# Performance work log

Hardware: AMD Instinct MI355X
Metric: run time of the kernel (lower is better)

Reference implementation:

```python
import jax, jax.numpy as jnp
import numpy as np

N_NODES = 100000
N_EDGES = 1600000
N_GRAPHS = 64
D_IN = 3
HIDDEN = 256
N_CLASSES = 10
NEG_SLOPE = 0.01  # torch F.leaky_relu default


def gcn_conv(x, W, b, src, dst, n_nodes):
    """GCNConv: D^{-1/2}(A+I)D^{-1/2} X W + b with self-loops."""
    h = x @ W  # [N, H]
    ones = jnp.ones(src.shape[0], h.dtype)
    deg = jax.ops.segment_sum(ones, dst, num_segments=n_nodes) + 1.0  # +1 self-loop
    dinv = jax.lax.rsqrt(deg)
    coef = dinv[src] * dinv[dst]  # [E]
    agg = jax.ops.segment_sum(h[src] * coef[:, None], dst, num_segments=n_nodes)
    agg = agg + h * (1.0 / deg)[:, None]  # self-loop contribution (norm = 1/deg)
    return agg + b


def leaky_relu(v):
    return jnp.where(v >= 0, v, NEG_SLOPE * v)


def setup_inputs() -> dict:
    key = jax.random.key(0)
    ks = jax.random.split(key, 12)
    x = jax.random.normal(ks[0], (N_NODES, D_IN), dtype=jnp.float32)
    edge_index = jax.random.randint(ks[1], (2, N_EDGES), 0, N_NODES, dtype=jnp.int32)
    batch = jnp.sort(jax.random.randint(ks[2], (N_NODES,), 0, N_GRAPHS, dtype=jnp.int32))
    s1 = 1.0 / np.sqrt(D_IN)
    s2 = 1.0 / np.sqrt(HIDDEN)
    W1 = jax.random.uniform(ks[3], (D_IN, HIDDEN), jnp.float32, -s1, s1)
    b1 = jnp.zeros((HIDDEN,), jnp.float32)
    W2 = jax.random.uniform(ks[4], (HIDDEN, HIDDEN), jnp.float32, -s2, s2)
    b2 = jnp.zeros((HIDDEN,), jnp.float32)
    W3 = jax.random.uniform(ks[5], (HIDDEN, HIDDEN), jnp.float32, -s2, s2)
    b3 = jnp.zeros((HIDDEN,), jnp.float32)
    Wc = jax.random.uniform(ks[6], (HIDDEN, N_CLASSES), jnp.float32, -s2, s2)
    bc = jax.random.uniform(ks[7], (N_CLASSES,), jnp.float32, -s2, s2)
    return {"x": x, "edge_index": edge_index, "batch": batch,
            "W1": W1, "b1": b1, "W2": W2, "b2": b2, "W3": W3, "b3": b3,
            "Wc": Wc, "bc": bc}


def reference(x, edge_index, batch, W1, b1, W2, b2, W3, b3, Wc, bc):
    src, dst = edge_index[0], edge_index[1]
    h = leaky_relu(gcn_conv(x, W1, b1, src, dst, N_NODES))
    h = leaky_relu(gcn_conv(h, W2, b2, src, dst, N_NODES))
    h = leaky_relu(gcn_conv(h, W3, b3, src, dst, N_NODES))
    # global mean pool over graphs
    sums = jax.ops.segment_sum(h, batch, num_segments=N_GRAPHS)
    cnt = jax.ops.segment_sum(jnp.ones((N_NODES,), h.dtype), batch, num_segments=N_GRAPHS)
    pooled = sums / jnp.maximum(cnt, 1.0)[:, None]  # [G, H]
    logits = pooled @ Wc + bc
    return jax.nn.softmax(logits, axis=1)
```

## Files before the change

### kernel.cpp

```cpp
#include <hip/hip_runtime.h>
#include <hip/hip_bf16.h>
#include <hip/hip_fp16.h>
#include <cstdint>
#include <cstddef>

#define N_NODES   100000
#define N_EDGES   1600000
#define N_GRAPHS  64
#define HIDDEN    256
#define N_CLASSES 10
#define NEG_SLOPE 0.01f

#define E_PAD    (N_EDGES + 8 * N_NODES)
#define GEMM_BLOCKS 391

#define PART_EDGES  8192
#define PART_BLOCKS ((N_EDGES + PART_EDGES - 1) / PART_EDGES)
#define SUB_BITS 10
#define SUB_SIZE 1024
#define N_SUB    ((N_NODES + SUB_SIZE - 1) / SUB_SIZE)
#define CAP_SUB  17408

typedef __attribute__((ext_vector_type(4))) float f32x4;
typedef __attribute__((ext_vector_type(2))) float f32x2;

__device__ __forceinline__ float bf2f(unsigned short u) {
    return __uint_as_float(((unsigned int)u) << 16);
}

__device__ __forceinline__ unsigned char f2fp8(float v) {
    return (unsigned char)(__builtin_amdgcn_cvt_pk_fp8_f32(v, v, 0, false) & 0xff);
}

__device__ __forceinline__ unsigned int rec_pack(int s, float c) {
    __half h = __float2half(c);
    unsigned short hb = reinterpret_cast<const __half_raw*>(&h)->x;
    return ((unsigned int)hb << 17) | (unsigned int)s;
}
__device__ __forceinline__ float rec_coef(unsigned int u) {
    __half_raw hr; hr.x = (unsigned short)(u >> 17);
    return __half2float(*reinterpret_cast<const __half*>(&hr));
}

__global__ __launch_bounds__(256) void k_partition(const int* __restrict__ src, const int* __restrict__ dst,
                                                   int* __restrict__ gcur, unsigned int* __restrict__ bucket) {
    __shared__ int lcnt[N_SUB];
    __shared__ int lbase[N_SUB];
    __shared__ int gbase[N_SUB];
    __shared__ unsigned int stage[PART_EDGES];
    int tid = threadIdx.x;
    for (int i = tid; i < N_SUB; i += 256) lcnt[i] = 0;
    __syncthreads();
    int e0 = blockIdx.x * PART_EDGES + tid * 8;
    for (int g = 0; g < 4; ++g) {
        int e = e0 + g * 2048;
        if (e < N_EDGES) {
            int4 da = *(const int4*)(dst + e);
            int4 db = *(const int4*)(dst + e + 4);
            int d[8] = {da.x, da.y, da.z, da.w, db.x, db.y, db.z, db.w};
#pragma unroll
            for (int j = 0; j < 8; ++j) atomicAdd(&lcnt[d[j] >> SUB_BITS], 1);
        }
    }
    __syncthreads();
    if (tid == 0) {
        int s = 0;
        for (int r = 0; r < N_SUB; ++r) { lbase[r] = s; s += lcnt[r]; }
    }
    __syncthreads();
    for (int i = tid; i < N_SUB; i += 256) {
        gbase[i] = atomicAdd(&gcur[i * 16], lcnt[i]);
        lcnt[i] = lbase[i];
    }
    __syncthreads();
    for (int g = 0; g < 4; ++g) {
        int e = e0 + g * 2048;
        if (e < N_EDGES) {
            int4 da = *(const int4*)(dst + e);
            int4 db = *(const int4*)(dst + e + 4);
            int4 sa = *(const int4*)(src + e);
            int4 sb = *(const int4*)(src + e + 4);
            int d[8] = {da.x, da.y, da.z, da.w, db.x, db.y, db.z, db.w};
            int s[8] = {sa.x, sa.y, sa.z, sa.w, sb.x, sb.y, sb.z, sb.w};
#pragma unroll
            for (int j = 0; j < 8; ++j) {
                int r = d[j] >> SUB_BITS;
                int p = atomicAdd(&lcnt[r], 1);
                stage[p] = ((unsigned int)(d[j] & (SUB_SIZE - 1)) << 17) | (unsigned int)s[j];
            }
        }
    }
    __syncthreads();
    int wv = tid >> 6, ln = tid & 63;
    for (int r = wv; r < N_SUB; r += 4) {
        int base = lbase[r], n = lcnt[r] - base, gb = gbase[r];
        unsigned int* dp = bucket + (size_t)r * CAP_SUB + gb;
        for (int k = ln; k < n; k += 64) dp[k] = stage[base + k];
    }
}

__global__ __launch_bounds__(512) void k_hist3(const unsigned int* __restrict__ bucket,
                                               const int* __restrict__ gcur, int* __restrict__ cnt) {
    int sub = blockIdx.x;
    __shared__ int hist[SUB_SIZE];
    for (int i = threadIdx.x; i < SUB_SIZE; i += 512) hist[i] = 0;
    __syncthreads();
    int n = gcur[sub * 16];
    const unsigned int* bp = bucket + (size_t)sub * CAP_SUB;
    for (int i0 = threadIdx.x * 8; i0 < n; i0 += 512 * 8) {
        uint4 ua = *(const uint4*)(bp + i0);
        uint4 ub = *(const uint4*)(bp + i0 + 4);
        unsigned int u[8] = {ua.x, ua.y, ua.z, ua.w, ub.x, ub.y, ub.z, ub.w};
        int m = n - i0; if (m > 8) m = 8;
#pragma unroll
        for (int j = 0; j < 8; ++j) if (j < m) atomicAdd(&hist[u[j] >> 17], 1);
    }
    __syncthreads();
    int base = sub * SUB_SIZE;
    for (int i = threadIdx.x; i < SUB_SIZE; i += 512)
        if (base + i < N_NODES) cnt[base + i] = hist[i];
}

__global__ __launch_bounds__(512) void k_fill3(const unsigned int* __restrict__ bucket,
                                               const int* __restrict__ gcur,
                                               const float* __restrict__ dinv,
                                               const int* __restrict__ off,
                                               unsigned int* __restrict__ rec) {
    int sub = blockIdx.x;
    __shared__ int lcur[SUB_SIZE];
    __shared__ float ldv[SUB_SIZE];
    int nb0 = sub * SUB_SIZE;
    for (int i = threadIdx.x; i < SUB_SIZE; i += 512) {
        int node = nb0 + i;
        lcur[i] = (node < N_NODES) ? off[node] : 0;
        ldv[i]  = (node < N_NODES) ? dinv[node] : 0.f;
    }
    __syncthreads();
    int n = gcur[sub * 16];
    const unsigned int* bp = bucket + (size_t)sub * CAP_SUB;
    for (int i0 = threadIdx.x * 8; i0 < n; i0 += 512 * 8) {
        uint4 ua = *(const uint4*)(bp + i0);
        uint4 ub = *(const uint4*)(bp + i0 + 4);
        unsigned int u[8] = {ua.x, ua.y, ua.z, ua.w, ub.x, ub.y, ub.z, ub.w};
        int m = n - i0; if (m > 8) m = 8;
        float ds[8];
#pragma unroll
        for (int j = 0; j < 8; ++j) {
            int s = (j < m) ? (int)(u[j] & 0x1ffff) : 0;
            ds[j] = dinv[s];
        }
#pragma unroll
        for (int j = 0; j < 8; ++j) {
            if (j < m) {
                int dr = (int)(u[j] >> 17);
                float c = ds[j] * ldv[dr];
                int p = atomicAdd(&lcur[dr], 1);
                rec[p] = rec_pack((int)(u[j] & 0x1ffff), c);
            }
        }
    }
}

__global__ void k_graph_bounds(const int* __restrict__ batch,
                               int* __restrict__ gstart, int* __restrict__ gcnt) {
    int g = threadIdx.x;
    int lo = 0, hi = N_NODES;
    while (lo < hi) { int mid = (lo + hi) >> 1; if (batch[mid] < g) lo = mid + 1; else hi = mid; }
    __shared__ int sh[N_GRAPHS + 1];
    sh[g] = lo;
    if (g == 0) sh[N_GRAPHS] = N_NODES;
    __syncthreads();
    gstart[g] = sh[g];
    gcnt[g]   = sh[g + 1] - sh[g];
}

__global__ void k_dinv_xpad(const int* __restrict__ cnt, const float* __restrict__ x,
                            float* __restrict__ dinv, float4* __restrict__ xp) {
    int i = blockIdx.x * 256 + threadIdx.x;
    if (i < N_NODES) {
        dinv[i] = rsqrtf((float)cnt[i] + 1.0f);
        xp[i] = make_float4(x[i * 3 + 0], x[i * 3 + 1], x[i * 3 + 2], 0.f);
    }
}

__global__ void k_scanA(const int* __restrict__ cnt, int* __restrict__ out, int* __restrict__ bsum) {
    __shared__ int sh[256];
    int tid = threadIdx.x;
    int base = blockIdx.x * 1024 + tid * 4;
    int v[4]; int s = 0;
#pragma unroll
    for (int i = 0; i < 4; i++) {
        int idx = base + i;
        v[i] = (idx < N_NODES) ? ((cnt[idx] + 7) & ~7) : 0;
        s += v[i];
    }
    sh[tid] = s; __syncthreads();
    for (int off = 1; off < 256; off <<= 1) {
        int t = (tid >= off) ? sh[tid - off] : 0;
        __syncthreads();
        sh[tid] += t;
        __syncthreads();
    }
    int excl = sh[tid] - s;
    if (tid == 255) bsum[blockIdx.x] = sh[255];
#pragma unroll
    for (int i = 0; i < 4; i++) { int idx = base + i; if (idx < N_NODES) out[idx] = excl; excl += v[i]; }
}

__global__ void k_scanB(int* __restrict__ bsum, int nb) {
    __shared__ int sh[128];
    int tid = threadIdx.x;
    int v = (tid < nb) ? bsum[tid] : 0;
    sh[tid] = v; __syncthreads();
    for (int off = 1; off < 128; off <<= 1) {
        int t = (tid >= off) ? sh[tid - off] : 0;
        __syncthreads();
        sh[tid] += t;
        __syncthreads();
    }
    if (tid < nb) bsum[tid] = sh[tid] - v;
}

__global__ void k_scanC(int* __restrict__ off_arr, const int* __restrict__ bsum,
                        const int* __restrict__ cnt, unsigned int* __restrict__ rec) {
    int i = blockIdx.x * 256 + threadIdx.x;
    if (i < N_NODES) {
        int v = off_arr[i] + bsum[i >> 10];
        off_arr[i] = v;
        int c  = cnt[i];
        int cp = (c + 7) & ~7;
        for (int p = v + c; p < v + cp; ++p) rec[p] = 0u;
        if (i == N_NODES - 1) off_arr[N_NODES] = v + cp;
    }
}

__global__ void k_wprep(const float* __restrict__ W, unsigned char* __restrict__ Wswz) {
    int n = blockIdx.x; int k = threadIdx.x;
    unsigned char v = f2fp8(W[k * HIDDEN + n]);
    int k0 = k >> 5, nt = n >> 4;
    int lane = (((k >> 3) & 3) << 4) | (n & 15);
    int j = k & 7;
    Wswz[(size_t)(((k0 * 16) + nt) * 64 + lane) * 8 + j] = v;
}

__global__ void k_agg3(const float4* __restrict__ xp, const int* __restrict__ off,
                       const unsigned int* __restrict__ rec, const float* __restrict__ dinv,
                       float4* __restrict__ ax) {
    int i = blockIdx.x * 256 + threadIdx.x;
    if (i >= N_NODES) return;
    float di = dinv[i];
    float selfc = di * di;
    float4 xi = xp[i];
    float a0 = xi.x * selfc, a1 = xi.y * selfc, a2 = xi.z * selfc;
    int e = off[i], e1 = off[i + 1];
    for (; e < e1; e += 4) {
        uint4 rr = *(const uint4*)(rec + e);
        int s0 = rr.x & 0x1ffff, s1 = rr.y & 0x1ffff, s2 = rr.z & 0x1ffff, s3 = rr.w & 0x1ffff;
        float c0 = rec_coef(rr.x), c1 = rec_coef(rr.y), c2 = rec_coef(rr.z), c3 = rec_coef(rr.w);
        float4 x0 = xp[s0], x1 = xp[s1], x2 = xp[s2], x3 = xp[s3];
        a0 += c0 * x0.x + c1 * x1.x + c2 * x2.x + c3 * x3.x;
        a1 += c0 * x0.y + c1 * x1.y + c2 * x2.y + c3 * x3.y;
        a2 += c0 * x0.z + c1 * x1.z + c2 * x2.z + c3 * x3.z;
    }
    ax[i] = make_float4(a0, a1, a2, 0.f);
}

__global__ void k_l1(const float4* __restrict__ ax, const float* __restrict__ W1,
                     const float* __restrict__ b1, unsigned char* __restrict__ out) {
    int node = blockIdx.x; int c = threadIdx.x;
    float4 a = ax[node];
    float v = a.x * W1[c] + a.y * W1[HIDDEN + c] + a.z * W1[2 * HIDDEN + c] + b1[c];
    v = v >= 0.f ? v : NEG_SLOPE * v;
    out[(size_t)node * HIDDEN + c] = f2fp8(v);
}

__global__ __launch_bounds__(512, 2) void k_gemm_mfma(const unsigned char* __restrict__ A,
                                                      const unsigned char* __restrict__ Wswz,
                                                      unsigned char* __restrict__ C, int M) {
    __shared__ long Bs[8192];
    __shared__ unsigned int St[8][320];
    int tid = threadIdx.x;
    {
        const float4* gsrc = (const float4*)Wswz;
        float4* ldst = (float4*)Bs;
#pragma unroll
        for (int i = 0; i < 8; ++i) ldst[tid + 512 * i] = gsrc[tid + 512 * i];
    }
    __syncthreads();
    int lane = tid & 63, wv = tid >> 6;
    int quad = lane >> 4, r = lane & 15;
    int nstrips = M >> 4;
    unsigned int* stw = &St[wv][0];
    int rrow = lane >> 2, rseg = lane & 3;
    for (int s = blockIdx.x * 8 + wv; s < nstrips; s += GEMM_BLOCKS * 8) {
        int m0 = s * 16;
        const long* Ab = (const long*)(A + (size_t)(m0 + r) * HIDDEN) + quad;
        long af[8];
#pragma unroll
        for (int k0 = 0; k0 < 8; ++k0) af[k0] = Ab[k0 * 4];
        f32x4 acc[16];
#pragma unroll
        for (int i = 0; i < 16; i++) acc[i] = (f32x4){0.f, 0.f, 0.f, 0.f};
#pragma unroll
        for (int k0 = 0; k0 < 8; ++k0) {
#pragma unroll
            for (int nt = 0; nt < 16; ++nt) {
                long w = Bs[(k0 * 16 + nt) * 64 + lane];
                acc[nt] = __builtin_amdgcn_mfma_f32_16x16x32_fp8_fp8(w, af[k0], acc[nt], 0, 0, 0);
            }
        }
#pragma unroll
        for (int q4 = 0; q4 < 4; ++q4) {
#pragma unroll
            for (int t = 0; t < 4; ++t) {
                f32x4 a = acc[q4 * 4 + t];
                unsigned int pk = __builtin_amdgcn_cvt_pk_fp8_f32(a[0], a[1], 0, false);
                pk = __builtin_amdgcn_cvt_pk_fp8_f32(a[2], a[3], pk, true);
                stw[r * 20 + t * 4 + quad] = pk;
            }
            uint4 v = *(const uint4*)&stw[rrow * 20 + rseg * 4];
            *(uint4*)(C + (size_t)(m0 + rrow) * HIDDEN + q4 * 64 + rseg * 16) = v;
        }
    }
}

__global__ __launch_bounds__(256) void k_agg(const unsigned char* __restrict__ h,
                                             const float* __restrict__ bias,
                                             const int* __restrict__ off, const unsigned int* __restrict__ rec,
                                             const float* __restrict__ dinv,
                                             unsigned char* __restrict__ out) {
    int node = (blockIdx.x * 256 + threadIdx.x) >> 6;
    int lane = threadIdx.x & 63;
    if (node >= N_NODES) return;
    float di = dinv[node];
    float selfc = di * di;
    unsigned int hv = *(const unsigned int*)(h + (size_t)node * HIDDEN + lane * 4);
    f32x2 hlo = __builtin_amdgcn_cvt_pk_f32_fp8(hv, false);
    f32x2 hhi = __builtin_amdgcn_cvt_pk_f32_fp8(hv, true);
    float4 bv = ((const float4*)bias)[lane];
    float4 acc = make_float4(bv.x + hlo.x * selfc, bv.y + hlo.y * selfc,
                             bv.z + hhi.x * selfc, bv.w + hhi.y * selfc);
    int e = off[node], e1 = off[node + 1];
    for (; e < e1; e += 8) {
        uint4 ra = *(const uint4*)(rec + e);
        uint4 rb = *(const uint4*)(rec + e + 4);
        unsigned int w0 = *(const unsigned int*)(h + (size_t)(ra.x & 0x1ffff) * HIDDEN + lane * 4);
        unsigned int w1 = *(const unsigned int*)(h + (size_t)(ra.y & 0x1ffff) * HIDDEN + lane * 4);
        unsigned int w2 = *(const unsigned int*)(h + (size_t)(ra.z & 0x1ffff) * HIDDEN + lane * 4);
        unsigned int w3 = *(const unsigned int*)(h + (size_t)(ra.w & 0x1ffff) * HIDDEN + lane * 4);
        unsigned int w4 = *(const unsigned int*)(h + (size_t)(rb.x & 0x1ffff) * HIDDEN + lane * 4);
        unsigned int w5 = *(const unsigned int*)(h + (size_t)(rb.y & 0x1ffff) * HIDDEN + lane * 4);
        unsigned int w6 = *(const unsigned int*)(h + (size_t)(rb.z & 0x1ffff) * HIDDEN + lane * 4);
        unsigned int w7 = *(const unsigned int*)(h + (size_t)(rb.w & 0x1ffff) * HIDDEN + lane * 4);
        float c0 = rec_coef(ra.x), c1 = rec_coef(ra.y), c2 = rec_coef(ra.z), c3 = rec_coef(ra.w);
        float c4 = rec_coef(rb.x), c5 = rec_coef(rb.y), c6 = rec_coef(rb.z), c7 = rec_coef(rb.w);
        f32x2 l0 = __builtin_amdgcn_cvt_pk_f32_fp8(w0, false), g0 = __builtin_amdgcn_cvt_pk_f32_fp8(w0, true);
        f32x2 l1 = __builtin_amdgcn_cvt_pk_f32_fp8(w1, false), g1 = __builtin_amdgcn_cvt_pk_f32_fp8(w1, true);
        f32x2 l2 = __builtin_amdgcn_cvt_pk_f32_fp8(w2, false), g2 = __builtin_amdgcn_cvt_pk_f32_fp8(w2, true);
        f32x2 l3 = __builtin_amdgcn_cvt_pk_f32_fp8(w3, false), g3 = __builtin_amdgcn_cvt_pk_f32_fp8(w3, true);
        f32x2 l4 = __builtin_amdgcn_cvt_pk_f32_fp8(w4, false), g4 = __builtin_amdgcn_cvt_pk_f32_fp8(w4, true);
        f32x2 l5 = __builtin_amdgcn_cvt_pk_f32_fp8(w5, false), g5 = __builtin_amdgcn_cvt_pk_f32_fp8(w5, true);
        f32x2 l6 = __builtin_amdgcn_cvt_pk_f32_fp8(w6, false), g6 = __builtin_amdgcn_cvt_pk_f32_fp8(w6, true);
        f32x2 l7 = __builtin_amdgcn_cvt_pk_f32_fp8(w7, false), g7 = __builtin_amdgcn_cvt_pk_f32_fp8(w7, true);
        acc.x += c0 * l0.x + c1 * l1.x + c2 * l2.x + c3 * l3.x
               + c4 * l4.x + c5 * l5.x + c6 * l6.x + c7 * l7.x;
        acc.y += c0 * l0.y + c1 * l1.y + c2 * l2.y + c3 * l3.y
               + c4 * l4.y + c5 * l5.y + c6 * l6.y + c7 * l7.y;
        acc.z += c0 * g0.x + c1 * g1.x + c2 * g2.x + c3 * g3.x
               + c4 * g4.x + c5 * g5.x + c6 * g6.x + c7 * g7.x;
        acc.w += c0 * g0.y + c1 * g1.y + c2 * g2.y + c3 * g3.y
               + c4 * g4.y + c5 * g5.y + c6 * g6.y + c7 * g7.y;
    }
    acc.x = acc.x >= 0.f ? acc.x : NEG_SLOPE * acc.x;
    acc.y = acc.y >= 0.f ? acc.y : NEG_SLOPE * acc.y;
    acc.z = acc.z >= 0.f ? acc.z : NEG_SLOPE * acc.z;
    acc.w = acc.w >= 0.f ? acc.w : NEG_SLOPE * acc.w;
    unsigned int pk = __builtin_amdgcn_cvt_pk_fp8_f32(acc.x, acc.y, 0, false);
    pk = __builtin_amdgcn_cvt_pk_fp8_f32(acc.z, acc.w, pk, true);
    *(unsigned int*)(out + (size_t)node * HIDDEN + lane * 4) = pk;
}

__global__ void k_pool(const unsigned char* __restrict__ h, const int* __restrict__ gstart,
                       const int* __restrict__ gcnt, float* __restrict__ pooled) {
    int g = blockIdx.x, chunk = blockIdx.y, t = threadIdx.x;
    int s = gstart[g], c = gcnt[g];
    int i0 = s + (int)(((long long)c * chunk) / 16);
    int i1 = s + (int)(((long long)c * (chunk + 1)) / 16);
    float acc = 0.f;
    for (int i = i0; i < i1; ++i) {
        f32x2 v = __builtin_amdgcn_cvt_pk_f32_fp8((unsigned int)h[(size_t)i * HIDDEN + t], false);
        acc += v.x;
    }
    atomicAdd(&pooled[g * HIDDEN + t], acc);
}

__global__ void k_head(const float* __restrict__ pooled, const int* __restrict__ gcnt,
                       const float* __restrict__ Wc, const float* __restrict__ bc,
                       float* __restrict__ out) {
    int g = blockIdx.x; int l = threadIdx.x;
    float inv = 1.0f / fmaxf((float)gcnt[g], 1.0f);
    float p[4];
#pragma unroll
    for (int i = 0; i < 4; i++) p[i] = pooled[g * HIDDEN + l + i * 64] * inv;
    __shared__ float logits[N_CLASSES];
#pragma unroll
    for (int j = 0; j < N_CLASSES; j++) {
        float s = 0.f;
#pragma unroll
        for (int i = 0; i < 4; i++) s += p[i] * Wc[(l + i * 64) * N_CLASSES + j];
        for (int o = 32; o > 0; o >>= 1) s += __shfl_down(s, o, 64);
        if (l == 0) logits[j] = s + bc[j];
    }
    __syncthreads();
    if (l == 0) {
        float m = logits[0];
        for (int j = 1; j < N_CLASSES; j++) m = fmaxf(m, logits[j]);
        float e[N_CLASSES]; float sum = 0.f;
        for (int j = 0; j < N_CLASSES; j++) { e[j] = expf(logits[j] - m); sum += e[j]; }
        for (int j = 0; j < N_CLASSES; j++) out[g * N_CLASSES + j] = e[j] / sum;
    }
}

extern "C" void kernel_launch(void* const* d_in, const int* in_sizes, int n_in,
                              void* d_out, int out_size, void* d_ws, size_t ws_size,
                              hipStream_t stream) {
    const float* x     = (const float*)d_in[0];
    const int*   edge  = (const int*)d_in[1];
    const int*   batch = (const int*)d_in[2];
    const float* W1 = (const float*)d_in[3];
    const float* b1 = (const float*)d_in[4];
    const float* W2 = (const float*)d_in[5];
    const float* b2 = (const float*)d_in[6];
    const float* W3 = (const float*)d_in[7];
    const float* b3 = (const float*)d_in[8];
    const float* Wc = (const float*)d_in[9];
    const float* bc = (const float*)d_in[10];
    float* out = (float*)d_out;
    const int* srcp = edge;
    const int* dstp = edge + N_EDGES;

    char* ws = (char*)d_ws;
    size_t off = 0;
    auto alloc = [&](size_t bytes) -> char* {
        char* p = ws + off;
        off += (bytes + 255) & ~(size_t)255;
        return p;
    };
    unsigned char* hA   = (unsigned char*)alloc((size_t)N_NODES * HIDDEN);
    unsigned char* hB   = (unsigned char*)alloc((size_t)N_NODES * HIDDEN);
    unsigned char* Wz2  = (unsigned char*)alloc((size_t)HIDDEN * HIDDEN);
    unsigned char* Wz3  = (unsigned char*)alloc((size_t)HIDDEN * HIDDEN);
    int*   deg_cnt  = (int*)alloc((size_t)N_NODES * 4);
    float* dinv     = (float*)alloc((size_t)N_NODES * 4);
    int*   csr_off  = (int*)alloc((size_t)(N_NODES + 1) * 4);
    unsigned int* csr_rec = (unsigned int*)alloc((size_t)E_PAD * 4);
    float4* ax      = (float4*)alloc((size_t)N_NODES * 16);
    float4* xp      = (float4*)alloc((size_t)N_NODES * 16);
    int*   gcnt     = (int*)alloc((size_t)N_GRAPHS * 4);
    int*   gstart   = (int*)alloc((size_t)N_GRAPHS * 4);
    float* pooled   = (float*)alloc((size_t)N_GRAPHS * HIDDEN * 4);
    int*   bsum     = (int*)alloc(128 * 4);
    int*   gcur     = (int*)alloc((size_t)N_SUB * 16 * 4);

    unsigned int* bucket = (unsigned int*)hB;

    hipMemsetAsync(gcur, 0, (size_t)N_SUB * 16 * 4, stream);
    hipMemsetAsync(pooled, 0, (size_t)N_GRAPHS * HIDDEN * 4, stream);

    int nb  = (N_NODES + 255) / 256;
    int sblocks = (N_NODES + 1023) / 1024;

    k_partition<<<PART_BLOCKS, 256, 0, stream>>>(srcp, dstp, gcur, bucket);
    k_graph_bounds<<<1, 64, 0, stream>>>(batch, gstart, gcnt);
    k_hist3<<<N_SUB, 512, 0, stream>>>(bucket, gcur, deg_cnt);
    k_dinv_xpad<<<nb, 256, 0, stream>>>(deg_cnt, x, dinv, xp);
    k_scanA<<<sblocks, 256, 0, stream>>>(deg_cnt, csr_off, bsum);
    k_scanB<<<1, 128, 0, stream>>>(bsum, sblocks);
    k_scanC<<<nb, 256, 0, stream>>>(csr_off, bsum, deg_cnt, csr_rec);
    k_fill3<<<N_SUB, 512, 0, stream>>>(bucket, gcur, dinv, csr_off, csr_rec);
    k_wprep<<<HIDDEN, HIDDEN, 0, stream>>>(W2, Wz2);
    k_wprep<<<HIDDEN, HIDDEN, 0, stream>>>(W3, Wz3);

    k_agg3<<<nb, 256, 0, stream>>>(xp, csr_off, csr_rec, dinv, ax);
    k_l1<<<N_NODES, 256, 0, stream>>>(ax, W1, b1, hA);

    int aggb = (N_NODES + 3) / 4;
    k_gemm_mfma<<<GEMM_BLOCKS, 512, 0, stream>>>(hA, Wz2, hB, N_NODES);
    k_agg<<<aggb, 256, 0, stream>>>(hB, b2, csr_off, csr_rec, dinv, hA);
    k_gemm_mfma<<<GEMM_BLOCKS, 512, 0, stream>>>(hA, Wz3, hB, N_NODES);
    k_agg<<<aggb, 256, 0, stream>>>(hB, b3, csr_off, csr_rec, dinv, hA);
    dim3 pg(N_GRAPHS, 16);
    k_pool<<<pg, 256, 0, stream>>>(hA, gstart, gcnt, pooled);
    k_head<<<N_GRAPHS, 64, 0, stream>>>(pooled, gcnt, Wc, bc, out);
}
```

Before: 455.7 us.

## Fuse dinv/xpad into hist, degree-sort layer-1 aggregation, batch k_l1 and wprep

Folds the dinv and padded-x computation into the histogram kernel and merges the two weight-prep launches into one, removing launches. Adds a per-1024-node counting sort by degree so the first-layer aggregation threads in a wavefront have similar edge counts, which is meant to reduce divergence. It also rewrites k_l1 to handle 32 nodes per block with W1 and b1 staged in shared memory instead of one block per node. The cost is an extra sort kernel and a perm array, plus scattered writes to ax.

```diff
diff --git a/kernel.cpp b/kernel.cpp
--- a/kernel.cpp
+++ b/kernel.cpp
@@ -100,7 +100,9 @@
 }
 
 __global__ __launch_bounds__(512) void k_hist3(const unsigned int* __restrict__ bucket,
-                                               const int* __restrict__ gcur, int* __restrict__ cnt) {
+                                               const int* __restrict__ gcur, int* __restrict__ cnt,
+                                               const float* __restrict__ x,
+                                               float* __restrict__ dinv, float4* __restrict__ xp) {
     int sub = blockIdx.x;
     __shared__ int hist[SUB_SIZE];
     for (int i = threadIdx.x; i < SUB_SIZE; i += 512) hist[i] = 0;
@@ -117,8 +119,44 @@
     }
     __syncthreads();
     int base = sub * SUB_SIZE;
-    for (int i = threadIdx.x; i < SUB_SIZE; i += 512)
-        if (base + i < N_NODES) cnt[base + i] = hist[i];
+    for (int i = threadIdx.x; i < SUB_SIZE; i += 512) {
+        int node = base + i;
+        if (node < N_NODES) {
+            int c = hist[i];
+            cnt[node] = c;
+            dinv[node] = rsqrtf((float)c + 1.0f);
+            xp[node] = make_float4(x[node * 3 + 0], x[node * 3 + 1], x[node * 3 + 2], 0.f);
+        }
+    }
+}
+
+__global__ __launch_bounds__(512) void k_locsort(const int* __restrict__ cnt, int* __restrict__ perm) {
+    int sub = blockIdx.x, t = threadIdx.x;
+    __shared__ int hist[256];
+    __shared__ int curs[256];
+    if (t < 256) hist[t] = 0;
+    __syncthreads();
+    int base = sub * SUB_SIZE;
+    int i0 = base + t, i1 = base + t + 512;
+    int d0 = -1, d1 = -1;
+    if (i0 < N_NODES) { d0 = min(cnt[i0], 254); atomicAdd(&hist[d0], 1); }
+    if (i1 < N_NODES) { d1 = min(cnt[i1], 254); atomicAdd(&hist[d1], 1); }
+    __syncthreads();
+    if (t < 256) curs[t] = hist[t];
+    __syncthreads();
+    for (int off = 1; off < 256; off <<= 1) {
+        int v = 0;
+        if (t < 256 && t >= off) v = curs[t - off];
+        __syncthreads();
+        if (t < 256) curs[t] += v;
+        __syncthreads();
+    }
+    if (t < 256) curs[t] -= hist[t];
+    __syncthreads();
+    if (d0 >= 0) { int p = atomicAdd(&curs[d0], 1); perm[base + p] = i0; }
+    if (d1 >= 0) { int p = atomicAdd(&curs[d1], 1); perm[base + p] = i1; }
+    int nvalid = N_NODES - base; if (nvalid > SUB_SIZE) nvalid = SUB_SIZE;
+    for (int k = nvalid + t; k < SUB_SIZE; k += 512) perm[base + k] = 0x7fffffff;
 }
 
 __global__ __launch_bounds__(512) void k_fill3(const unsigned int* __restrict__ bucket,
@@ -174,15 +212,6 @@
     gcnt[g]   = sh[g + 1] - sh[g];
 }
 
-__global__ void k_dinv_xpad(const int* __restrict__ cnt, const float* __restrict__ x,
-                            float* __restrict__ dinv, float4* __restrict__ xp) {
-    int i = blockIdx.x * 256 + threadIdx.x;
-    if (i < N_NODES) {
-        dinv[i] = rsqrtf((float)cnt[i] + 1.0f);
-        xp[i] = make_float4(x[i * 3 + 0], x[i * 3 + 1], x[i * 3 + 2], 0.f);
-    }
-}
-
 __global__ void k_scanA(const int* __restrict__ cnt, int* __restrict__ out, int* __restrict__ bsum) {
     __shared__ int sh[256];
     int tid = threadIdx.x;
@@ -234,7 +263,10 @@
     }
 }
 
-__global__ void k_wprep(const float* __restrict__ W, unsigned char* __restrict__ Wswz) {
+__global__ void k_wprep2(const float* __restrict__ W2, const float* __restrict__ W3,
+                         unsigned char* __restrict__ Wz2, unsigned char* __restrict__ Wz3) {
+    const float* W = blockIdx.y ? W3 : W2;
+    unsigned char* Wswz = blockIdx.y ? Wz3 : Wz2;
     int n = blockIdx.x; int k = threadIdx.x;
     unsigned char v = f2fp8(W[k * HIDDEN + n]);
     int k0 = k >> 5, nt = n >> 4;
@@ -245,8 +277,9 @@
 
 __global__ void k_agg3(const float4* __restrict__ xp, const int* __restrict__ off,
                        const unsigned int* __restrict__ rec, const float* __restrict__ dinv,
-                       float4* __restrict__ ax) {
-    int i = blockIdx.x * 256 + threadIdx.x;
+                       const int* __restrict__ perm, float4* __restrict__ ax) {
+    int gid = blockIdx.x * 256 + threadIdx.x;
+    int i = perm[gid];
     if (i >= N_NODES) return;
     float di = dinv[i];
     float selfc = di * di;
@@ -265,13 +298,22 @@
     ax[i] = make_float4(a0, a1, a2, 0.f);
 }
 
-__global__ void k_l1(const float4* __restrict__ ax, const float* __restrict__ W1,
-                     const float* __restrict__ b1, unsigned char* __restrict__ out) {
-    int node = blockIdx.x; int c = threadIdx.x;
-    float4 a = ax[node];
-    float v = a.x * W1[c] + a.y * W1[HIDDEN + c] + a.z * W1[2 * HIDDEN + c] + b1[c];
-    v = v >= 0.f ? v : NEG_SLOPE * v;
-    out[(size_t)node * HIDDEN + c] = f2fp8(v);
+__global__ __launch_bounds__(256) void k_l1(const float4* __restrict__ ax, const float* __restrict__ W1,
+                                            const float* __restrict__ b1, unsigned char* __restrict__ out) {
+    __shared__ float w0s[HIDDEN], w1s[HIDDEN], w2s[HIDDEN], bbs[HIDDEN];
+    int t = threadIdx.x;
+    w0s[t] = W1[t]; w1s[t] = W1[HIDDEN + t]; w2s[t] = W1[2 * HIDDEN + t]; bbs[t] = b1[t];
+    __syncthreads();
+    int base = blockIdx.x * 32;
+#pragma unroll 4
+    for (int i = 0; i < 32; ++i) {
+        int node = base + i;
+        if (node >= N_NODES) break;
+        float4 a = ax[node];
+        float v = a.x * w0s[t] + a.y * w1s[t] + a.z * w2s[t] + bbs[t];
+        v = v >= 0.f ? v : NEG_SLOPE * v;
+        out[(size_t)node * HIDDEN + t] = f2fp8(v);
+    }
 }
 
 __global__ __launch_bounds__(512, 2) void k_gemm_mfma(const unsigned char* __restrict__ A,
@@ -461,6 +503,7 @@
     float* pooled   = (float*)alloc((size_t)N_GRAPHS * HIDDEN * 4);
     int*   bsum     = (int*)alloc(128 * 4);
     int*   gcur     = (int*)alloc((size_t)N_SUB * 16 * 4);
+    int*   perm     = (int*)alloc((size_t)N_SUB * SUB_SIZE * 4);
 
     unsigned int* bucket = (unsigned int*)hB;
 
@@ -472,17 +515,17 @@
 
     k_partition<<<PART_BLOCKS, 256, 0, stream>>>(srcp, dstp, gcur, bucket);
     k_graph_bounds<<<1, 64, 0, stream>>>(batch, gstart, gcnt);
-    k_hist3<<<N_SUB, 512, 0, stream>>>(bucket, gcur, deg_cnt);
-    k_dinv_xpad<<<nb, 256, 0, stream>>>(deg_cnt, x, dinv, xp);
+    k_hist3<<<N_SUB, 512, 0, stream>>>(bucket, gcur, deg_cnt, x, dinv, xp);
+    k_locsort<<<N_SUB, 512, 0, stream>>>(deg_cnt, perm);
     k_scanA<<<sblocks, 256, 0, stream>>>(deg_cnt, csr_off, bsum);
     k_scanB<<<1, 128, 0, stream>>>(bsum, sblocks);
     k_scanC<<<nb, 256, 0, stream>>>(csr_off, bsum, deg_cnt, csr_rec);
     k_fill3<<<N_SUB, 512, 0, stream>>>(bucket, gcur, dinv, csr_off, csr_rec);
-    k_wprep<<<HIDDEN, HIDDEN, 0, stream>>>(W2, Wz2);
-    k_wprep<<<HIDDEN, HIDDEN, 0, stream>>>(W3, Wz3);
-
-    k_agg3<<<nb, 256, 0, stream>>>(xp, csr_off, csr_rec, dinv, ax);
-    k_l1<<<N_NODES, 256, 0, stream>>>(ax, W1, b1, hA);
+    dim3 wg(HIDDEN, 2);
+    k_wprep2<<<wg, HIDDEN, 0, stream>>>(W2, W3, Wz2, Wz3);
+
+    k_agg3<<<(N_SUB * SUB_SIZE) / 256, 256, 0, stream>>>(xp, csr_off, csr_rec, dinv, perm, ax);
+    k_l1<<<(N_NODES + 31) / 32, 256, 0, stream>>>(ax, W1, b1, hA);
 
     int aggb = (N_NODES + 3) / 4;
     k_gemm_mfma<<<GEMM_BLOCKS, 512, 0, stream>>>(hA, Wz2, hB, N_NODES);
```

New measurement: 449.6 us. About the same (-1.3%).
